# Optimization experiments

Hardware: AMD Instinct MI355X
Metric: run time of the kernel (lower is better)

Reference implementation:

```python
import jax, jax.numpy as jnp
import numpy as np

N = 50000        # nodes
E = 800000       # edges (before self-loops)
A_DIM = 128      # attribute dim (= a_hid)
S_DIM = 64       # structural dim (= s_hid)
L = 4            # num_layers


def setup_inputs() -> dict:
    key = jax.random.key(0)
    ks = jax.random.split(key, 10)
    sc = 0.05
    return {
        "x": jax.random.normal(ks[0], (N, A_DIM), jnp.float32),
        "s": jax.random.normal(ks[1], (N, S_DIM), jnp.float32),
        "edge_index": jax.random.randint(ks[2], (2, E), 0, N, dtype=jnp.int64),
        "gcn_W": jax.random.normal(ks[3], (L, A_DIM, A_DIM), jnp.float32) * sc,
        "gcn_b": jnp.zeros((L, A_DIM), jnp.float32),
        "gna_w1W": jax.random.normal(ks[4], (L, S_DIM, S_DIM), jnp.float32) * sc,
        "gna_w1b": jnp.zeros((L, S_DIM), jnp.float32),
        "gna_w2W": jax.random.normal(ks[5], (L, S_DIM, S_DIM), jnp.float32) * sc,
        "gna_w2b": jnp.zeros((L, S_DIM), jnp.float32),
        "gna_a": jax.random.normal(ks[6], (L, S_DIM), jnp.float32) * sc,
    }


def _gelu(v):
    return jax.nn.gelu(v, approximate=False)  # matches torch F.gelu default


def _self_loops(edge_index, n):
    loop = jnp.arange(n, dtype=edge_index.dtype)
    row = jnp.concatenate([edge_index[0], loop])  # src
    col = jnp.concatenate([edge_index[1], loop])  # dst
    return row, col


def _guide_forward(x, s, edge_index, gcn_W, gcn_b,
                   gna_w1W, gna_w1b, gna_w2W, gna_w2b, gna_a):
    n = x.shape[0]
    row, col = _self_loops(edge_index, n)  # [E+N]

    # ---- attribute autoencoder: GCN with symmetric normalization ----
    deg = jax.ops.segment_sum(jnp.ones_like(col, dtype=x.dtype), col, num_segments=n)
    dinv = jnp.where(deg > 0, jax.lax.rsqrt(deg), 0.0)
    norm = dinv[row] * dinv[col]                       # [E+N]
    h = x
    for i in range(L):
        h2 = h @ gcn_W[i]                              # [N, A]
        agg = jax.ops.segment_sum(norm[:, None] * h2[row], col, num_segments=n)
        h = agg + gcn_b[i]
        if i < L - 1:                                  # jk=None: no act after last
            h = _gelu(h)

    # ---- structure autoencoder: GNA with edge-softmax attention ----
    g = s
    for i in range(L):
        t = g @ gna_w2W[i] + gna_w2b[i]                # w2(s), [N, S]
        # alpha_e = (t_dst - t_src) @ a, softmax over edges grouped by dst
        alpha = (t[col] - t[row]) @ gna_a[i]           # [E+N]
        amax = jax.ops.segment_max(alpha, col, num_segments=n)
        e = jnp.exp(alpha - amax[col])
        denom = jax.ops.segment_sum(e, col, num_segments=n)
        w = e / (denom[col] + 1e-16)
        msg = jax.ops.segment_sum(w[:, None] * t[row], col, num_segments=n)
        out = g @ gna_w1W[i] + gna_w1b[i] + msg
        g = _gelu(out)                                 # act applied after every layer
    return h, g


def reference(x, s, edge_index, gcn_W, gcn_b,
              gna_w1W, gna_w1b, gna_w2W, gna_w2b, gna_a):
    return _guide_forward(x, s, edge_index, gcn_W, gcn_b,
                          gna_w1W, gna_w1b, gna_w2W, gna_w2b, gna_a)
```

## Files before the change

kernel.cpp:

```cpp
#include <hip/hip_runtime.h>
#include <hip/hip_fp16.h>
#include <math.h>

#define N_NODES 50000
#define E_EDGES 800000
#define ET (E_EDGES + N_NODES)
#define L_LAYERS 4
#define NB_SCAN ((N_NODES + 255) / 256)
#define MF2_BLOCKS ((N_NODES + 127) / 128)
#define WAVE_BLOCKS ((N_NODES * 64 + 255) / 256)

typedef __attribute__((ext_vector_type(8))) short short8;
typedef __attribute__((ext_vector_type(4))) float f32x4;

__device__ __forceinline__ float gelu_f(float x) {
    float z = fabsf(x) * 0.70710678118654752f;
    float t = __fdividef(1.0f, fmaf(0.3275911f, z, 1.0f));
    float p = t * fmaf(t, fmaf(t, fmaf(t, fmaf(t, 1.061405429f, -1.453152027f),
                                       1.421413741f), -0.284496736f),
                       0.254829592f);
    float e = __expf(-z * z);
    float erfz = copysignf(fmaf(-p, e, 1.0f), x);
    return 0.5f * x * (1.0f + erfz);
}

__device__ __forceinline__ void split_hl(float x, unsigned short& h, unsigned short& lo) {
    unsigned u = __float_as_uint(x);
    h = (unsigned short)(u >> 16);
    float hif = __uint_as_float(u & 0xffff0000u);
    lo = (unsigned short)(__float_as_uint(x - hif) >> 16);
}

__device__ __forceinline__ void fma8h(const float4& raw, float m, float* acc) {
    const __half2* h = reinterpret_cast<const __half2*>(&raw);
#pragma unroll
    for (int i = 0; i < 4; ++i) {
        float2 f = __half22float2(h[i]);
        acc[2 * i]     = fmaf(f.x, m, acc[2 * i]);
        acc[2 * i + 1] = fmaf(f.y, m, acc[2 * i + 1]);
    }
}


__global__ __launch_bounds__(256) void count_pos(const int* __restrict__ ecol,
                                                 int* __restrict__ cnt,
                                                 int* __restrict__ aux) {
    int e = blockIdx.x * 256 + threadIdx.x;
    if (e >= ET) return;
    int c = (e < E_EDGES) ? ecol[e] : (e - E_EDGES);
    aux[e] = atomicAdd(&cnt[c], 1);
}

__global__ __launch_bounds__(256) void scan_part1(const int* __restrict__ cnt,
                                                  int* __restrict__ bsum) {
    __shared__ int red[256];
    int t = threadIdx.x;
    int i = blockIdx.x * 256 + t;
    red[t] = (i < N_NODES) ? cnt[i] : 0;
    __syncthreads();
#pragma unroll
    for (int off = 128; off; off >>= 1) {
        if (t < off) red[t] += red[t + off];
        __syncthreads();
    }
    if (t == 0) bsum[blockIdx.x] = red[0];
}

__global__ __launch_bounds__(256) void scan_part3(const int* __restrict__ cnt,
                                                  const int* __restrict__ bsum,
                                                  int* __restrict__ ptrb,
                                                  float* __restrict__ dinv) {
    __shared__ int red[256];
    __shared__ int sh[256];
    int t = threadIdx.x;
    red[t] = (t < (int)blockIdx.x) ? bsum[t] : 0;
    __syncthreads();
#pragma unroll
    for (int off = 128; off; off >>= 1) {
        if (t < off) red[t] += red[t + off];
        __syncthreads();
    }
    int base = red[0];
    int i = blockIdx.x * 256 + t;
    int v = (i < N_NODES) ? cnt[i] : 0;
    sh[t] = v;
    __syncthreads();
    for (int off = 1; off < 256; off <<= 1) {
        int u = (t >= off) ? sh[t - off] : 0;
        __syncthreads();
        sh[t] += u;
        __syncthreads();
    }
    int excl = sh[t] - v + base;
    if (i < N_NODES) {
        ptrb[i] = excl;
        dinv[i] = rsqrtf((float)v);
    }
    if (i == N_NODES - 1) ptrb[N_NODES] = excl + v;
}

__global__ __launch_bounds__(256) void bucket(const int* __restrict__ erow,
                                              const int* __restrict__ ecol,
                                              const int* __restrict__ aux,
                                              const int* __restrict__ ptrb,
                                              int* __restrict__ eidx) {
    int e = blockIdx.x * 256 + threadIdx.x;
    if (e >= ET) return;
    int r, c;
    if (e < E_EDGES) { r = erow[e]; c = ecol[e]; }
    else             { r = e - E_EDGES; c = r; }
    int pos = ptrb[c] + aux[e];
    eidx[pos] = r;
}


__global__ __launch_bounds__(256) void prep_w(const float* __restrict__ gcn_W,
                                              const float* __restrict__ w1W,
                                              const float* __restrict__ w2W,
                                              unsigned short* __restrict__ gf_hi,
                                              unsigned short* __restrict__ gf_lo,
                                              unsigned short* __restrict__ nf_hi,
                                              unsigned short* __restrict__ nf_lo) {
    int idx = blockIdx.x * 256 + threadIdx.x;
    if (idx < 8192) {
        int lane = idx & 63, nt = (idx >> 6) & 7, s = (idx >> 9) & 3, layer = idx >> 11;
        int q = lane >> 4, n = lane & 15;
        const float* W = gcn_W + (size_t)layer * 128 * 128;
        size_t o = (size_t)idx * 8;
#pragma unroll
        for (int j = 0; j < 8; ++j) {
            float x = W[(size_t)(s * 32 + q * 8 + j) * 128 + nt * 16 + n];
            unsigned short h, lo;
            split_hl(x, h, lo);
            gf_hi[o + j] = h; gf_lo[o + j] = lo;
        }
    } else if (idx < 8192 + 4096) {
        int t = idx - 8192;
        int lane = t & 63, nt = (t >> 6) & 7, s = (t >> 9) & 1, layer = t >> 10;
        int q = lane >> 4, n = lane & 15;
        int col = nt * 16 + n;
        const float* W = (col < 64) ? (w1W + (size_t)layer * 64 * 64)
                                    : (w2W + (size_t)layer * 64 * 64);
        int c = col & 63;
        size_t o = (size_t)t * 8;
#pragma unroll
        for (int j = 0; j < 8; ++j) {
            float x = W[(size_t)(s * 32 + q * 8 + j) * 64 + c];
            unsigned short h, lo;
            split_hl(x, h, lo);
            nf_hi[o + j] = h; nf_lo[o + j] = lo;
        }
    }
}


__device__ __forceinline__ void mfma_steps2(const float* __restrict__ A, int Kfull,
                                            int nsteps,
                                            const unsigned short* __restrict__ wfh,
                                            const unsigned short* __restrict__ wfl,
                                            const int* arow, const bool* avalid,
                                            int lq, int l, f32x4 acc[2][8]) {
    for (int s = 0; s < nsteps; ++s) {
        short8 ah[2], al[2];
#pragma unroll
        for (int g = 0; g < 2; ++g) {
            float4 a0 = make_float4(0.f, 0.f, 0.f, 0.f);
            float4 a1 = make_float4(0.f, 0.f, 0.f, 0.f);
            if (avalid[g]) {
                const float* ap = A + (size_t)arow[g] * Kfull + s * 32 + lq * 8;
                a0 = *(const float4*)ap;
                a1 = *(const float4*)(ap + 4);
            }
            float xs[8] = {a0.x, a0.y, a0.z, a0.w, a1.x, a1.y, a1.z, a1.w};
#pragma unroll
            for (int c = 0; c < 8; ++c) {
                unsigned short h, lo;
                split_hl(xs[c], h, lo);
                ah[g][c] = (short)h; al[g][c] = (short)lo;
            }
        }
#pragma unroll
        for (int nt = 0; nt < 8; ++nt) {
            size_t fo = ((size_t)(s * 8 + nt) * 64 + l) * 8;
            short8 wh = *(const short8*)(wfh + fo);
            short8 wl = *(const short8*)(wfl + fo);
#pragma unroll
            for (int g = 0; g < 2; ++g) {
                acc[g][nt] = __builtin_amdgcn_mfma_f32_16x16x32_bf16(ah[g], wh, acc[g][nt], 0, 0, 0);
                acc[g][nt] = __builtin_amdgcn_mfma_f32_16x16x32_bf16(ah[g], wl, acc[g][nt], 0, 0, 0);
                acc[g][nt] = __builtin_amdgcn_mfma_f32_16x16x32_bf16(al[g], wh, acc[g][nt], 0, 0, 0);
            }
        }
    }
}


__global__ __launch_bounds__(256) void gemm_both(
    const float* __restrict__ A0, const float* __restrict__ A1,
    const unsigned short* __restrict__ gfh, const unsigned short* __restrict__ gfl,
    const unsigned short* __restrict__ nfh, const unsigned short* __restrict__ nfl,
    const float* __restrict__ b1, const float* __restrict__ b2,
    const float* __restrict__ avec, const float* __restrict__ dinv,
    __half* __restrict__ h2, float* __restrict__ baseb,
    __half* __restrict__ ut, float* __restrict__ ub) {
    int tid = threadIdx.x;
    int w  = tid >> 6;
    int l  = tid & 63;
    int lq = l >> 4;
    int ln = l & 15;
    bool isg = blockIdx.x >= MF2_BLOCKS;
    int blk = isg ? (blockIdx.x - MF2_BLOCKS) : blockIdx.x;
    int m0 = blk * 128;
    int arow[2];
    bool avalid[2];
#pragma unroll
    for (int g = 0; g < 2; ++g) {
        arow[g] = m0 + w * 32 + g * 16 + ln;
        avalid[g] = arow[g] < N_NODES;
    }

    f32x4 acc[2][8];
#pragma unroll
    for (int g = 0; g < 2; ++g)
#pragma unroll
        for (int i = 0; i < 8; ++i) acc[g][i] = (f32x4){0.f, 0.f, 0.f, 0.f};

    if (!isg) {
        mfma_steps2(A0, 128, 4, gfh, gfl, arow, avalid, lq, l, acc);
#pragma unroll
        for (int g = 0; g < 2; ++g) {
            float dv[4];
#pragma unroll
            for (int r = 0; r < 4; ++r) {
                int row = m0 + w * 32 + g * 16 + lq * 4 + r;
                dv[r] = (row < N_NODES) ? dinv[row] : 0.f;
            }
#pragma unroll
            for (int nt = 0; nt < 8; ++nt) {
                int col = nt * 16 + ln;
#pragma unroll
                for (int r = 0; r < 4; ++r) {
                    int row = m0 + w * 32 + g * 16 + lq * 4 + r;
                    if (row < N_NODES)
                        h2[(size_t)row * 128 + col] = __float2half(acc[g][nt][r] * dv[r]);
                }
            }
        }
    } else {
        mfma_steps2(A1, 64, 2, nfh, nfl, arow, avalid, lq, l, acc);
#pragma unroll
        for (int g = 0; g < 2; ++g) {
#pragma unroll
            for (int nt = 0; nt < 4; ++nt) {
                int col = nt * 16 + ln;
                float bb = b1[col];
#pragma unroll
                for (int r = 0; r < 4; ++r) {
                    int row = m0 + w * 32 + g * 16 + lq * 4 + r;
                    if (row < N_NODES) baseb[(size_t)row * 64 + col] = acc[g][nt][r] + bb;
                }
            }
            float pa[4] = {0.f, 0.f, 0.f, 0.f};
            float t2s[4][4];
#pragma unroll
            for (int nt = 4; nt < 8; ++nt) {
                int col = (nt - 4) * 16 + ln;
                float bb = b2[col];
                float av = avec[col];
#pragma unroll
                for (int r = 0; r < 4; ++r) {
                    float t2 = acc[g][nt][r] + bb;
                    t2s[nt - 4][r] = t2;
                    pa[r] += t2 * av;
                }
            }
#pragma unroll
            for (int r = 0; r < 4; ++r) {
                pa[r] += __shfl_xor(pa[r], 1);
                pa[r] += __shfl_xor(pa[r], 2);
                pa[r] += __shfl_xor(pa[r], 4);
                pa[r] += __shfl_xor(pa[r], 8);
            }
            float ur[4];
#pragma unroll
            for (int r = 0; r < 4; ++r) ur[r] = expf(-pa[r]);
#pragma unroll
            for (int nt = 0; nt < 4; ++nt) {
                int col = nt * 16 + ln;
#pragma unroll
                for (int r = 0; r < 4; ++r) {
                    int row = m0 + w * 32 + g * 16 + lq * 4 + r;
                    if (row < N_NODES)
                        ut[(size_t)row * 64 + col] = __float2half(t2s[nt][r] * ur[r]);
                }
            }
            if (ln == 0) {
#pragma unroll
                for (int r = 0; r < 4; ++r) {
                    int row = m0 + w * 32 + g * 16 + lq * 4 + r;
                    if (row < N_NODES) ub[row] = ur[r];
                }
            }
        }
    }
}


__global__ __launch_bounds__(256) void agg_gcn(const __half* __restrict__ h2,
                                               const int* __restrict__ ptrb,
                                               const int* __restrict__ eidx,
                                               const float* __restrict__ dinv,
                                               const float* __restrict__ bias,
                                               float* __restrict__ out,
                                               int apply_gelu) {
    int dst  = (blockIdx.x * 256 + threadIdx.x) >> 6;
    int lane = threadIdx.x & 63;
    if (dst >= N_NODES) return;
    int sub = lane >> 4;
    int fl  = lane & 15;
    int p0 = ptrb[dst], p1 = ptrb[dst + 1];
    float acc[8];
#pragma unroll
    for (int i = 0; i < 8; ++i) acc[i] = 0.f;
    for (int p = p0; p < p1; p += 64) {
        int nb = min(64, p1 - p);
        int srcs = (lane < nb) ? eidx[p + lane] : 0;
        for (int eb = 0; eb < nb; eb += 16) {
            int   sv[4];
            float mk[4];
#pragma unroll
            for (int k = 0; k < 4; ++k) {
                int e = eb + sub + 4 * k;
                int c = min(e, nb - 1);
                sv[k] = __shfl(srcs, c);
                mk[k] = (e < nb) ? 1.f : 0.f;
            }
            float4 raw[4];
#pragma unroll
            for (int k = 0; k < 4; ++k)
                raw[k] = *(const float4*)(h2 + (size_t)sv[k] * 128 + fl * 8);
#pragma unroll
            for (int k = 0; k < 4; ++k) fma8h(raw[k], mk[k], acc);
        }
    }
#pragma unroll
    for (int off = 16; off <= 32; off <<= 1)
#pragma unroll
        for (int i = 0; i < 8; ++i) acc[i] += __shfl_xor(acc[i], off);
    {
        float dd = dinv[dst];
        int c0 = fl * 8 + 2 * sub;
        float2 bb = *(const float2*)(bias + c0);
        float v0 = fmaf(dd, acc[2 * sub], bb.x);
        float v1 = fmaf(dd, acc[2 * sub + 1], bb.y);
        if (apply_gelu) { v0 = gelu_f(v0); v1 = gelu_f(v1); }
        *(float2*)(out + (size_t)dst * 128 + c0) = make_float2(v0, v1);
    }
}


__global__ __launch_bounds__(256) void gna_agg(const __half* __restrict__ ut,
                                               const float* __restrict__ ub,
                                               const int* __restrict__ ptrb,
                                               const int* __restrict__ eidx,
                                               const float* __restrict__ base,
                                               float* __restrict__ gout) {
    int dst  = (blockIdx.x * 256 + threadIdx.x) >> 6;
    int lane = threadIdx.x & 63;
    if (dst >= N_NODES) return;
    int p0 = ptrb[dst], p1 = ptrb[dst + 1];
    int sub = lane >> 3;
    int fl  = lane & 7;
    float se = 0.f;
    float acc[8];
#pragma unroll
    for (int i = 0; i < 8; ++i) acc[i] = 0.f;
    for (int p = p0; p < p1; p += 64) {
        int nb = min(64, p1 - p);
        int srcs = (lane < nb) ? eidx[p + lane] : 0;
        if (lane < nb) se += ub[srcs];
        for (int eb = 0; eb < nb; eb += 32) {
            int   sv[4];
            float mk[4];
#pragma unroll
            for (int k = 0; k < 4; ++k) {
                int e = eb + sub + 8 * k;
                int c = min(e, nb - 1);
                sv[k] = __shfl(srcs, c);
                mk[k] = (e < nb) ? 1.f : 0.f;
            }
            float4 raw[4];
#pragma unroll
            for (int k = 0; k < 4; ++k)
                raw[k] = *(const float4*)(ut + (size_t)sv[k] * 64 + fl * 8);
#pragma unroll
            for (int k = 0; k < 4; ++k) fma8h(raw[k], mk[k], acc);
        }
    }
#pragma unroll
    for (int off = 1; off < 64; off <<= 1) se += __shfl_xor(se, off);
#pragma unroll
    for (int off = 8; off <= 32; off <<= 1)
#pragma unroll
        for (int i = 0; i < 8; ++i) acc[i] += __shfl_xor(acc[i], off);
    {
        float winv = __fdividef(1.0f, se + 1e-16f);
        int c0 = fl * 8 + sub;
        float bs = base[(size_t)dst * 64 + c0];
        gout[(size_t)dst * 64 + c0] = gelu_f(fmaf(acc[sub], winv, bs));
    }
}


extern "C" void kernel_launch(void* const* d_in, const int* in_sizes, int n_in,
                              void* d_out, int out_size, void* d_ws, size_t ws_size,
                              hipStream_t stream) {
    const float* x     = (const float*)d_in[0];
    const float* s     = (const float*)d_in[1];
    const int*   ei    = (const int*)d_in[2];
    const float* gcn_W = (const float*)d_in[3];
    const float* gcn_b = (const float*)d_in[4];
    const float* w1W   = (const float*)d_in[5];
    const float* w1b   = (const float*)d_in[6];
    const float* w2W   = (const float*)d_in[7];
    const float* w2b   = (const float*)d_in[8];
    const float* ga    = (const float*)d_in[9];

    float* h_out = (float*)d_out;
    float* g_out = (float*)d_out + (size_t)N_NODES * 128;

    size_t off = 0;
    char* wsb = (char*)d_ws;
    auto take = [&](size_t bytes) {
        void* p = wsb + off;
        off = (off + bytes + 255) & ~(size_t)255;
        return p;
    };
    int*    cnt     = (int*)take((size_t)N_NODES * 4);
    int*    ptrb    = (int*)take((size_t)(N_NODES + 1) * 4);
    int*    aux     = (int*)take((size_t)ET * 4);
    float*  dinv    = (float*)take((size_t)N_NODES * 4);
    int*    eidx    = (int*)take((size_t)ET * 4);
    __half* h2      = (__half*)take((size_t)N_NODES * 128 * 2);
    __half* utbuf   = (__half*)take((size_t)N_NODES * 64 * 2);
    float*  basebuf = (float*)take((size_t)N_NODES * 64 * 4);
    float*  ubuf    = (float*)take((size_t)N_NODES * 4);
    int*    bsum    = (int*)take((size_t)NB_SCAN * 4);
    unsigned short* gf_hi = (unsigned short*)take((size_t)8192 * 8 * 2);
    unsigned short* gf_lo = (unsigned short*)take((size_t)8192 * 8 * 2);
    unsigned short* nf_hi = (unsigned short*)take((size_t)4096 * 8 * 2);
    unsigned short* nf_lo = (unsigned short*)take((size_t)4096 * 8 * 2);
    (void)ws_size; (void)in_sizes; (void)n_in; (void)out_size;

    const int* erow = ei;
    const int* ecol = ei + E_EDGES;

    hipMemsetAsync(cnt, 0, (size_t)N_NODES * 4, stream);

    int ge = (ET + 255) / 256;
    count_pos<<<ge, 256, 0, stream>>>(ecol, cnt, aux);
    scan_part1<<<NB_SCAN, 256, 0, stream>>>(cnt, bsum);
    scan_part3<<<NB_SCAN, 256, 0, stream>>>(cnt, bsum, ptrb, dinv);
    bucket<<<ge, 256, 0, stream>>>(erow, ecol, aux, ptrb, eidx);
    prep_w<<<48, 256, 0, stream>>>(gcn_W, w1W, w2W, gf_hi, gf_lo, nf_hi, nf_lo);

    const float* hin = x;
    const float* gin = s;
    for (int l = 0; l < L_LAYERS; ++l) {
        gemm_both<<<2 * MF2_BLOCKS, 256, 0, stream>>>(
            hin, gin,
            gf_hi + (size_t)l * 4 * 8 * 64 * 8, gf_lo + (size_t)l * 4 * 8 * 64 * 8,
            nf_hi + (size_t)l * 2 * 8 * 64 * 8, nf_lo + (size_t)l * 2 * 8 * 64 * 8,
            w1b + (size_t)l * 64, w2b + (size_t)l * 64, ga + (size_t)l * 64, dinv,
            h2, basebuf, utbuf, ubuf);
        agg_gcn<<<WAVE_BLOCKS, 256, 0, stream>>>(
            h2, ptrb, eidx, dinv, gcn_b + (size_t)l * 128, h_out,
            (l < L_LAYERS - 1) ? 1 : 0);
        gna_agg<<<WAVE_BLOCKS, 256, 0, stream>>>(
            utbuf, ubuf, ptrb, eidx, basebuf, g_out);
        hin = h_out;
        gin = g_out;
    }
}
```

Baseline: 489.3 us.

## Process two destination nodes per wavefront in GCN and GNA aggregation

Each 64-lane wavefront in the aggregation kernels now handles two destination nodes, one per 32-lane half, instead of one. Each lane gathers more edge rows per step (8 instead of 4), so more loads are in flight, and the cross-lane reduction shrinks. Outputs are written with wider float4/float2 stores. With an average degree near 17, the aim is to waste fewer masked lanes on low-degree nodes. The risk is load imbalance between the two halves when degrees differ, plus higher register pressure.

```diff
diff --git a/kernel.cpp b/kernel.cpp
--- a/kernel.cpp
+++ b/kernel.cpp
@@ -8,7 +8,7 @@
 #define L_LAYERS 4
 #define NB_SCAN ((N_NODES + 255) / 256)
 #define MF2_BLOCKS ((N_NODES + 127) / 128)
-#define WAVE_BLOCKS ((N_NODES * 64 + 255) / 256)
+#define AGG_BLOCKS ((N_NODES / 2 * 64 + 255) / 256)
 
 typedef __attribute__((ext_vector_type(8))) short short8;
 typedef __attribute__((ext_vector_type(4))) float f32x4;
@@ -313,48 +313,53 @@
                                                const float* __restrict__ bias,
                                                float* __restrict__ out,
                                                int apply_gelu) {
-    int dst  = (blockIdx.x * 256 + threadIdx.x) >> 6;
+    int widx = (blockIdx.x * 256 + (int)threadIdx.x) >> 6;
     int lane = threadIdx.x & 63;
+    int half = lane >> 5;
+    int hl   = lane & 31;
+    int dst  = widx * 2 + half;
     if (dst >= N_NODES) return;
-    int sub = lane >> 4;
-    int fl  = lane & 15;
+    int sub = hl >> 4;
+    int fl  = hl & 15;
     int p0 = ptrb[dst], p1 = ptrb[dst + 1];
     float acc[8];
 #pragma unroll
     for (int i = 0; i < 8; ++i) acc[i] = 0.f;
-    for (int p = p0; p < p1; p += 64) {
-        int nb = min(64, p1 - p);
-        int srcs = (lane < nb) ? eidx[p + lane] : 0;
+    for (int p = p0; p < p1; p += 32) {
+        int nb = min(32, p1 - p);
+        int srcs = (hl < nb) ? eidx[p + hl] : 0;
         for (int eb = 0; eb < nb; eb += 16) {
-            int   sv[4];
-            float mk[4];
-#pragma unroll
-            for (int k = 0; k < 4; ++k) {
-                int e = eb + sub + 4 * k;
-                int c = min(e, nb - 1);
+            int   sv[8];
+            float mk[8];
+#pragma unroll
+            for (int k = 0; k < 8; ++k) {
+                int e = eb + sub + 2 * k;
+                int c = half * 32 + min(e, nb - 1);
                 sv[k] = __shfl(srcs, c);
                 mk[k] = (e < nb) ? 1.f : 0.f;
             }
-            float4 raw[4];
-#pragma unroll
-            for (int k = 0; k < 4; ++k)
+            float4 raw[8];
+#pragma unroll
+            for (int k = 0; k < 8; ++k)
                 raw[k] = *(const float4*)(h2 + (size_t)sv[k] * 128 + fl * 8);
 #pragma unroll
-            for (int k = 0; k < 4; ++k) fma8h(raw[k], mk[k], acc);
-        }
-    }
-#pragma unroll
-    for (int off = 16; off <= 32; off <<= 1)
-#pragma unroll
-        for (int i = 0; i < 8; ++i) acc[i] += __shfl_xor(acc[i], off);
+            for (int k = 0; k < 8; ++k) fma8h(raw[k], mk[k], acc);
+        }
+    }
+#pragma unroll
+    for (int i = 0; i < 8; ++i) acc[i] += __shfl_xor(acc[i], 16);
     {
         float dd = dinv[dst];
-        int c0 = fl * 8 + 2 * sub;
-        float2 bb = *(const float2*)(bias + c0);
-        float v0 = fmaf(dd, acc[2 * sub], bb.x);
-        float v1 = fmaf(dd, acc[2 * sub + 1], bb.y);
-        if (apply_gelu) { v0 = gelu_f(v0); v1 = gelu_f(v1); }
-        *(float2*)(out + (size_t)dst * 128 + c0) = make_float2(v0, v1);
+        int c0 = fl * 8 + 4 * sub;
+        float4 bb = *(const float4*)(bias + c0);
+        float v0 = fmaf(dd, acc[4 * sub + 0], bb.x);
+        float v1 = fmaf(dd, acc[4 * sub + 1], bb.y);
+        float v2 = fmaf(dd, acc[4 * sub + 2], bb.z);
+        float v3 = fmaf(dd, acc[4 * sub + 3], bb.w);
+        if (apply_gelu) {
+            v0 = gelu_f(v0); v1 = gelu_f(v1); v2 = gelu_f(v2); v3 = gelu_f(v3);
+        }
+        *(float4*)(out + (size_t)dst * 128 + c0) = make_float4(v0, v1, v2, v3);
     }
 }
 
@@ -365,49 +370,52 @@
                                                const int* __restrict__ eidx,
                                                const float* __restrict__ base,
                                                float* __restrict__ gout) {
-    int dst  = (blockIdx.x * 256 + threadIdx.x) >> 6;
+    int widx = (blockIdx.x * 256 + (int)threadIdx.x) >> 6;
     int lane = threadIdx.x & 63;
+    int half = lane >> 5;
+    int hl   = lane & 31;
+    int dst  = widx * 2 + half;
     if (dst >= N_NODES) return;
+    int sub = hl >> 3;
+    int fl  = hl & 7;
     int p0 = ptrb[dst], p1 = ptrb[dst + 1];
-    int sub = lane >> 3;
-    int fl  = lane & 7;
     float se = 0.f;
     float acc[8];
 #pragma unroll
     for (int i = 0; i < 8; ++i) acc[i] = 0.f;
-    for (int p = p0; p < p1; p += 64) {
-        int nb = min(64, p1 - p);
-        int srcs = (lane < nb) ? eidx[p + lane] : 0;
-        if (lane < nb) se += ub[srcs];
-        for (int eb = 0; eb < nb; eb += 32) {
-            int   sv[4];
-            float mk[4];
-#pragma unroll
-            for (int k = 0; k < 4; ++k) {
-                int e = eb + sub + 8 * k;
-                int c = min(e, nb - 1);
-                sv[k] = __shfl(srcs, c);
-                mk[k] = (e < nb) ? 1.f : 0.f;
-            }
-            float4 raw[4];
-#pragma unroll
-            for (int k = 0; k < 4; ++k)
-                raw[k] = *(const float4*)(ut + (size_t)sv[k] * 64 + fl * 8);
-#pragma unroll
-            for (int k = 0; k < 4; ++k) fma8h(raw[k], mk[k], acc);
-        }
-    }
-#pragma unroll
-    for (int off = 1; off < 64; off <<= 1) se += __shfl_xor(se, off);
-#pragma unroll
-    for (int off = 8; off <= 32; off <<= 1)
+    for (int p = p0; p < p1; p += 32) {
+        int nb = min(32, p1 - p);
+        int srcs = (hl < nb) ? eidx[p + hl] : 0;
+        if (hl < nb) se += ub[srcs];
+        int   sv[8];
+        float mk[8];
+#pragma unroll
+        for (int k = 0; k < 8; ++k) {
+            int e = sub + 4 * k;
+            int c = half * 32 + min(e, nb - 1);
+            sv[k] = __shfl(srcs, c);
+            mk[k] = (e < nb) ? 1.f : 0.f;
+        }
+        float4 raw[8];
+#pragma unroll
+        for (int k = 0; k < 8; ++k)
+            raw[k] = *(const float4*)(ut + (size_t)sv[k] * 64 + fl * 8);
+#pragma unroll
+        for (int k = 0; k < 8; ++k) fma8h(raw[k], mk[k], acc);
+    }
+#pragma unroll
+    for (int off = 1; off <= 16; off <<= 1) se += __shfl_xor(se, off);
+#pragma unroll
+    for (int off = 8; off <= 16; off <<= 1)
 #pragma unroll
         for (int i = 0; i < 8; ++i) acc[i] += __shfl_xor(acc[i], off);
     {
         float winv = __fdividef(1.0f, se + 1e-16f);
-        int c0 = fl * 8 + sub;
-        float bs = base[(size_t)dst * 64 + c0];
-        gout[(size_t)dst * 64 + c0] = gelu_f(fmaf(acc[sub], winv, bs));
+        int c0 = fl * 8 + 2 * sub;
+        float2 bs = *(const float2*)(base + (size_t)dst * 64 + c0);
+        float v0 = gelu_f(fmaf(acc[2 * sub + 0], winv, bs.x));
+        float v1 = gelu_f(fmaf(acc[2 * sub + 1], winv, bs.y));
+        *(float2*)(gout + (size_t)dst * 64 + c0) = make_float2(v0, v1);
     }
 }
 
@@ -473,10 +481,10 @@
             nf_hi + (size_t)l * 2 * 8 * 64 * 8, nf_lo + (size_t)l * 2 * 8 * 64 * 8,
             w1b + (size_t)l * 64, w2b + (size_t)l * 64, ga + (size_t)l * 64, dinv,
             h2, basebuf, utbuf, ubuf);
-        agg_gcn<<<WAVE_BLOCKS, 256, 0, stream>>>(
+        agg_gcn<<<AGG_BLOCKS, 256, 0, stream>>>(
             h2, ptrb, eidx, dinv, gcn_b + (size_t)l * 128, h_out,
             (l < L_LAYERS - 1) ? 1 : 0);
-        gna_agg<<<WAVE_BLOCKS, 256, 0, stream>>>(
+        gna_agg<<<AGG_BLOCKS, 256, 0, stream>>>(
             utbuf, ubuf, ptrb, eidx, basebuf, g_out);
         hin = h_out;
         gin = g_out;
```

After: 480.1 us. No clear change (-1.9%).
